# Performance work log

Measured on AMD Instinct MI355X. Metric: run time of the kernel, lower is better.

Reference implementation:

```python
import jax, jax.numpy as jnp
import numpy as np

B, N, D, DC, R = 32, 36, 2048, 4, 512  # batch, regions, feat dim, coord dim, fusion rank


def setup_inputs() -> dict:
    key = jax.random.key(0)
    ks = jax.random.split(key, 8)
    s = lambda fan_in: 1.0 / np.sqrt(fan_in)
    return {
        "mm": jax.random.normal(ks[0], (B, N, D), dtype=jnp.float32),
        "coords": jax.random.uniform(ks[1], (B, N, DC), dtype=jnp.float32),
        "U_feat": jax.random.normal(ks[2], (D, R), dtype=jnp.float32) * s(D),
        "V_feat": jax.random.normal(ks[3], (D, R), dtype=jnp.float32) * s(D),
        "P_feat": jax.random.normal(ks[4], (R, D), dtype=jnp.float32) * s(R),
        "U_coord": jax.random.normal(ks[5], (DC, R), dtype=jnp.float32) * s(DC),
        "V_coord": jax.random.normal(ks[6], (DC, R), dtype=jnp.float32) * s(DC),
        "P_coord": jax.random.normal(ks[7], (R, D), dtype=jnp.float32) * s(R),
    }


def reference(mm, coords, U_feat, V_feat, P_feat, U_coord, V_coord, P_coord):
    # Pairwise module: build all (i, j) region pairs, fuse, max-aggregate over j.
    # Original torch code detach_()'s the gathered pair tensors -> stop_gradient here.
    mm_sg = jax.lax.stop_gradient(mm)
    coords_sg = jax.lax.stop_gradient(coords)

    # Coord fusion (MLB-style low-rank multiplicative fusion)
    uc = jnp.einsum("bnc,cr->bnr", coords_sg, U_coord)   # [B,N,R]
    vc = jnp.einsum("bnc,cr->bnr", coords_sg, V_coord)   # [B,N,R]
    zc = jax.nn.relu(uc[:, :, None, :] * vc[:, None, :, :])  # [B,N,N,R]
    Rij = jnp.einsum("bijr,rd->bijd", zc, P_coord)       # [B,N,N,D]

    # Feature fusion
    uf = jnp.einsum("bnd,dr->bnr", mm_sg, U_feat)
    vf = jnp.einsum("bnd,dr->bnr", mm_sg, V_feat)
    zf = jax.nn.relu(uf[:, :, None, :] * vf[:, None, :, :])  # [B,N,N,R]
    Rij = Rij + jnp.einsum("bijr,rd->bijd", zf, P_feat)  # [B,N,N,D]

    # agg['type'] == 'max': reduce over the second region axis (j)
    mm_new = jnp.max(Rij, axis=2)                        # [B,N,D]

    # residual
    return mm_new + mm
```

## Files before the change

kernel.cpp:

```cpp
#include <hip/hip_runtime.h>

#define BI    1152
#define NREG  36
#define DD    2048
#define RR    512
#define KK    1024
#define ZROWS (BI*NREG)
#define MBLK  144
#define NBLK  256
#define ABUF  (MBLK*32)
#define BBUF  (NBLK*32)
#define BUFE  (ABUF+BBUF)

typedef __bf16 bf16;
typedef __bf16 bf16x8 __attribute__((ext_vector_type(8)));
typedef __bf16 bf16x4 __attribute__((ext_vector_type(4)));
typedef float  f32x4  __attribute__((ext_vector_type(4)));

__device__ __forceinline__ void gl_lds16(const void* g, void* l) {
  __builtin_amdgcn_global_load_lds(
      (const __attribute__((address_space(1))) unsigned int*)g,
      (__attribute__((address_space(3))) unsigned int*)l, 16, 0, 0);
}

__global__ void k_prep(const float* __restrict__ mm, const float* __restrict__ coords,
                       const float* __restrict__ U_feat, const float* __restrict__ V_feat,
                       const float* __restrict__ P_feat, const float* __restrict__ U_coord,
                       const float* __restrict__ V_coord, const float* __restrict__ P_coord,
                       bf16* __restrict__ mmb, bf16* __restrict__ UT, bf16* __restrict__ VT,
                       bf16* __restrict__ PTt, float* __restrict__ uc, float* __restrict__ vc) {
  __shared__ float tile[32][33];
  int bid = blockIdx.x, tid = threadIdx.x;
  if (bid < 2304) {
    int i = bid * 256 + tid;
    float4 v = ((const float4*)mm)[i];
    bf16x4 o = {(bf16)v.x, (bf16)v.y, (bf16)v.z, (bf16)v.w};
    ((bf16x4*)mmb)[i] = o;
  } else if (bid < 4352) {
    int rel = bid - 2304;
    int zz = rel >> 10, rr = rel & 1023;
    int c0 = (rr & 15) * 32, r0 = (rr >> 4) * 32;
    const float* in = zz ? V_feat : U_feat;
    bf16* outp = zz ? VT : UT;
    int tx = tid & 31, ty = tid >> 5;
#pragma unroll
    for (int k = 0; k < 4; k++)
      tile[ty + 8 * k][tx] = in[(long)(r0 + ty + 8 * k) * 512 + c0 + tx];
    __syncthreads();
#pragma unroll
    for (int k = 0; k < 4; k++)
      outp[(long)(c0 + ty + 8 * k) * 2048 + r0 + tx] = (bf16)tile[tx][ty + 8 * k];
  } else if (bid < 6400) {
    int rel = bid - 4352;
    int zz = rel >> 10, rr = rel & 1023;
    int c0 = (rr & 63) * 32, r0 = (rr >> 6) * 32;
    const float* in = zz ? P_feat : P_coord;
    int koff = zz * 512;
    int tx = tid & 31, ty = tid >> 5;
#pragma unroll
    for (int k = 0; k < 4; k++)
      tile[ty + 8 * k][tx] = in[(long)(r0 + ty + 8 * k) * 2048 + c0 + tx];
    __syncthreads();
    int kc = (koff + r0) >> 5;
#pragma unroll
    for (int k = 0; k < 4; k++) {
      int d = c0 + ty + 8 * k;
      PTt[((long)kc * 2048 + d) * 32 + tx] = (bf16)tile[tx][ty + 8 * k];
    }
  } else {
    int g = bid - 6400;
    float c0 = coords[g * 4 + 0], c1 = coords[g * 4 + 1];
    float c2 = coords[g * 4 + 2], c3 = coords[g * 4 + 3];
#pragma unroll
    for (int i = 0; i < 2; i++) {
      int r = tid + i * 256;
      uc[g * RR + r] = c0 * U_coord[r] + c1 * U_coord[RR + r] + c2 * U_coord[2 * RR + r] + c3 * U_coord[3 * RR + r];
      vc[g * RR + r] = c0 * V_coord[r] + c1 * V_coord[RR + r] + c2 * V_coord[2 * RR + r] + c3 * V_coord[3 * RR + r];
    }
  }
}

__launch_bounds__(256)
__global__ void k_gemm_uv(const bf16* __restrict__ mmb, const bf16* __restrict__ UT,
                          const bf16* __restrict__ VT, float* __restrict__ uf,
                          float* __restrict__ vf) {
  __shared__ bf16 lds2[2][6144];
  const bf16* Bmat = blockIdx.z ? VT : UT;
  float* outp = blockIdx.z ? vf : uf;
  int m0 = blockIdx.x * 64, n0 = blockIdx.y * 128;
  int tid = threadIdx.x, wave = tid >> 6, lane = tid & 63;
  int l15 = lane & 15, qv = lane >> 4;
  int qp_c = qv ^ ((l15 >> 1) & 3);
  int qs = (lane & 3) ^ ((lane >> 3) & 3);

  const bf16* gA = mmb + (long)(m0 + wave * 16 + (lane >> 2)) * 2048 + qs * 8;
  const bf16* gB = Bmat + (long)(n0 + wave * 32 + (lane >> 2)) * 2048 + qs * 8;
  int lA = wave * 512;
  int lB = 2048 + wave * 1024;

  auto stage = [&](int buf, int k0) {
    bf16* db = &lds2[buf][0];
    gl_lds16(gA + k0, db + lA);
    gl_lds16(gB + k0, db + lB);
    gl_lds16(gB + 16 * 2048 + k0, db + lB + 512);
  };

  f32x4 acc[4][2] = {};
  stage(0, 0);
  for (int k0 = 0; k0 < 2048; k0 += 32) {
    int cur = (k0 >> 5) & 1;
    __syncthreads();
    if (k0 + 32 < 2048) stage(cur ^ 1, k0 + 32);
    bf16x8 a[4], b[2];
#pragma unroll
    for (int mt = 0; mt < 4; mt++)
      a[mt] = *(const bf16x8*)(&lds2[cur][0] + (mt * 16 + l15) * 32 + qp_c * 8);
#pragma unroll
    for (int nt = 0; nt < 2; nt++)
      b[nt] = *(const bf16x8*)(&lds2[cur][2048] + (wave * 32 + nt * 16 + l15) * 32 + qp_c * 8);
#pragma unroll
    for (int mt = 0; mt < 4; mt++)
#pragma unroll
      for (int nt = 0; nt < 2; nt++)
        acc[mt][nt] = __builtin_amdgcn_mfma_f32_16x16x32_bf16(a[mt], b[nt], acc[mt][nt], 0, 0, 0);
  }
#pragma unroll
  for (int mt = 0; mt < 4; mt++)
#pragma unroll
    for (int nt = 0; nt < 2; nt++)
#pragma unroll
      for (int r = 0; r < 4; r++) {
        int row = m0 + mt * 16 + qv * 4 + r;
        int col = n0 + wave * 32 + nt * 16 + l15;
        outp[(long)row * RR + col] = acc[mt][nt][r];
      }
}

__global__ void k_build_z(const float* __restrict__ uc, const float* __restrict__ vc,
                          const float* __restrict__ uf, const float* __restrict__ vf,
                          bf16* __restrict__ z) {
  __shared__ float uL[36 * 128];
  __shared__ float vL[36 * 128];
  int kq = blockIdx.x, b = blockIdx.y, tid = threadIdx.x;
  const float* usrc = (kq < 4) ? uc : uf;
  const float* vsrc = (kq < 4) ? vc : vf;
  int kb = (kq & 3) * 128;
  for (int i = tid; i < 1152; i += 256) {
    int row = i >> 5, kk = (i & 31) * 4;
    long src = (long)(b * 36 + row) * RR + kb + kk;
    *(float4*)&uL[row * 128 + kk] = *(const float4*)(usrc + src);
    *(float4*)&vL[row * 128 + kk] = *(const float4*)(vsrc + src);
  }
  __syncthreads();
  for (int c = tid; c < 41472; c += 256) {
    int kcl = c / 10368;
    int rem = c - kcl * 10368;
    int row = rem >> 3;
    int x4 = rem & 7;
    int gl = row / 36;
    int j = row - gl * 36;
    int kl = kcl * 32 + x4 * 4;
    float4 u4 = *(const float4*)&uL[gl * 128 + kl];
    float4 v4 = *(const float4*)&vL[j * 128 + kl];
    float x0 = fmaxf(u4.x * v4.x, 0.f), x1 = fmaxf(u4.y * v4.y, 0.f);
    float x2 = fmaxf(u4.z * v4.z, 0.f), x3 = fmaxf(u4.w * v4.w, 0.f);
    bf16x4 o = {(bf16)x0, (bf16)x1, (bf16)x2, (bf16)x3};
    int bi = b * 36 + gl;
    long rowp = (long)(bi >> 2) * 144 + j * 4 + (bi & 3);
    *(bf16x4*)(z + ((long)(kq * 4 + kcl) * ZROWS + rowp) * 32 + x4 * 4) = o;
  }
}

__launch_bounds__(256, 2)
__global__ void k_main(const bf16* __restrict__ z, const bf16* __restrict__ PTt,
                       const float* __restrict__ mm, float* __restrict__ out) {
  __shared__ bf16 lds[2 * BUFE];
  int bid = blockIdx.x;
  int x = bid & 7, t = bid >> 3;
  int dt = t & 7, go = (t >> 3) * 8 + x;
  int d0 = dt * NBLK;
  int tid = threadIdx.x, wave = tid >> 6, lane = tid & 63;
  int l15 = lane & 15, qv = lane >> 4;
  int qp_c = qv ^ ((l15 >> 1) & 3);

  int qs = (lane & 3) ^ ((lane >> 3) & 3);
  int lroff = (lane >> 2) * 32 + qs * 8;

  const bf16* gA = z + (long)go * ABUF + wave * 1024 + lroff;
  const bf16* gB = PTt + (long)d0 * 32 + wave * 2048 + lroff;
  int lA = wave * 1024;
  int lB = ABUF + wave * 2048;

  int sbuf = 0;
  auto stage = [&]() {
    bf16* db = lds + sbuf * BUFE;
    gl_lds16(gA, db + lA);
    gl_lds16(gA + 512, db + lA + 512);
    if (wave == 0) gl_lds16(gA + 4096, db + 4096);
    gl_lds16(gB, db + lB);
    gl_lds16(gB + 512, db + lB + 512);
    gl_lds16(gB + 1024, db + lB + 1024);
    gl_lds16(gB + 1536, db + lB + 1536);
    gA += (long)ZROWS * 32;
    gB += 2048L * 32;
    sbuf ^= 1;
  };

  f32x4 acc[9][4] = {};
  stage();
  for (int kc = 0; kc < 32; kc++) {
    __syncthreads();
    if (kc < 31) stage();
    const bf16* cur = lds + (kc & 1) * BUFE;
    bf16x8 b[4];
#pragma unroll
    for (int nt = 0; nt < 4; nt++)
      b[nt] = *(const bf16x8*)(cur + ABUF + (wave * 64 + nt * 16 + l15) * 32 + qp_c * 8);
#pragma unroll
    for (int mt = 0; mt < 9; mt++) {
      bf16x8 av = *(const bf16x8*)(cur + (mt * 16 + l15) * 32 + qp_c * 8);
#pragma unroll
      for (int nt = 0; nt < 4; nt++)
        acc[mt][nt] = __builtin_amdgcn_mfma_f32_16x16x32_bf16(av, b[nt], acc[mt][nt], 0, 0, 0);
    }
  }

#pragma unroll
  for (int nt = 0; nt < 4; nt++) {
    float mx[4];
#pragma unroll
    for (int r = 0; r < 4; r++) {
      mx[r] = acc[0][nt][r];
#pragma unroll
      for (int mt = 1; mt < 9; mt++) mx[r] = fmaxf(mx[r], acc[mt][nt][r]);
      mx[r] = fmaxf(mx[r], __shfl_xor(mx[r], 16, 64));
      mx[r] = fmaxf(mx[r], __shfl_xor(mx[r], 32, 64));
    }
    if (lane < 16) {
      int col = d0 + wave * 64 + nt * 16 + lane;
#pragma unroll
      for (int r = 0; r < 4; r++) {
        long oa = (long)(go * 4 + r) * DD + col;
        out[oa] = mx[r] + mm[oa];
      }
    }
  }
}

extern "C" void kernel_launch(void* const* d_in, const int* in_sizes, int n_in,
                              void* d_out, int out_size, void* d_ws, size_t ws_size,
                              hipStream_t stream) {
  const float* mm     = (const float*)d_in[0];
  const float* coords = (const float*)d_in[1];
  const float* U_feat = (const float*)d_in[2];
  const float* V_feat = (const float*)d_in[3];
  const float* P_feat = (const float*)d_in[4];
  const float* U_coord= (const float*)d_in[5];
  const float* V_coord= (const float*)d_in[6];
  const float* P_coord= (const float*)d_in[7];
  float* out = (float*)d_out;

  char* ws = (char*)d_ws;
  bf16* z   = (bf16*)(ws + 0);
  bf16* PTt = (bf16*)(ws + 84934656);
  bf16* mmb = (bf16*)(ws + 89128960);
  bf16* UT  = (bf16*)(ws + 93847552);
  bf16* VT  = (bf16*)(ws + 95944704);
  float* uf = (float*)(ws + 98041856);
  float* vf = (float*)(ws + 100401152);
  float* uc = (float*)(ws + 102760448);
  float* vc = (float*)(ws + 105119744);

  k_prep<<<dim3(7552), dim3(256), 0, stream>>>(mm, coords, U_feat, V_feat, P_feat,
                                               U_coord, V_coord, P_coord,
                                               mmb, UT, VT, PTt, uc, vc);
  k_gemm_uv<<<dim3(18, 4, 2), dim3(256), 0, stream>>>(mmb, UT, VT, uf, vf);
  k_build_z<<<dim3(8, 32), dim3(256), 0, stream>>>(uc, vc, uf, vf, z);
  k_main<<<dim3(2304), dim3(256), 0, stream>>>(z, PTt, mm, out);
}
```

Baseline: 259.7 us.

## Split-K uv GEMM, split z-build grid, load P operand directly to registers

The uv projection GEMM is split along K into two halves, which doubles its block count, and the partial sums are added when k_build_z loads them. k_build_z also gets a third grid dimension so each block writes half the z tiles. In k_main the B (P) operand is now read straight from global memory into registers instead of being staged through LDS, which cuts LDS use and LDS traffic. The cost is extra workspace and global reads for the partial sums, and B loads that go uncoalesced through the cache instead of through LDS.

Result: no change. 255.9 us (-1.5%).

```diff
diff --git a/kernel.cpp b/kernel.cpp
--- a/kernel.cpp
+++ b/kernel.cpp
@@ -9,8 +9,6 @@
 #define MBLK  144
 #define NBLK  256
 #define ABUF  (MBLK*32)
-#define BBUF  (NBLK*32)
-#define BUFE  (ABUF+BBUF)
 
 typedef __bf16 bf16;
 typedef __bf16 bf16x8 __attribute__((ext_vector_type(8)));
@@ -83,18 +81,21 @@
 __launch_bounds__(256)
 __global__ void k_gemm_uv(const bf16* __restrict__ mmb, const bf16* __restrict__ UT,
                           const bf16* __restrict__ VT, float* __restrict__ uf,
-                          float* __restrict__ vf) {
+                          float* __restrict__ vf, float* __restrict__ uf2,
+                          float* __restrict__ vf2) {
   __shared__ bf16 lds2[2][6144];
-  const bf16* Bmat = blockIdx.z ? VT : UT;
-  float* outp = blockIdx.z ? vf : uf;
+  int uv = blockIdx.z >> 1, kh = blockIdx.z & 1;
+  const bf16* Bmat = uv ? VT : UT;
+  float* outp = uv ? (kh ? vf2 : vf) : (kh ? uf2 : uf);
   int m0 = blockIdx.x * 64, n0 = blockIdx.y * 128;
+  int kbase = kh * 1024;
   int tid = threadIdx.x, wave = tid >> 6, lane = tid & 63;
   int l15 = lane & 15, qv = lane >> 4;
   int qp_c = qv ^ ((l15 >> 1) & 3);
   int qs = (lane & 3) ^ ((lane >> 3) & 3);
 
-  const bf16* gA = mmb + (long)(m0 + wave * 16 + (lane >> 2)) * 2048 + qs * 8;
-  const bf16* gB = Bmat + (long)(n0 + wave * 32 + (lane >> 2)) * 2048 + qs * 8;
+  const bf16* gA = mmb + (long)(m0 + wave * 16 + (lane >> 2)) * 2048 + kbase + qs * 8;
+  const bf16* gB = Bmat + (long)(n0 + wave * 32 + (lane >> 2)) * 2048 + kbase + qs * 8;
   int lA = wave * 512;
   int lB = 2048 + wave * 1024;
 
@@ -107,10 +108,10 @@
 
   f32x4 acc[4][2] = {};
   stage(0, 0);
-  for (int k0 = 0; k0 < 2048; k0 += 32) {
+  for (int k0 = 0; k0 < 1024; k0 += 32) {
     int cur = (k0 >> 5) & 1;
     __syncthreads();
-    if (k0 + 32 < 2048) stage(cur ^ 1, k0 + 32);
+    if (k0 + 32 < 1024) stage(cur ^ 1, k0 + 32);
     bf16x8 a[4], b[2];
 #pragma unroll
     for (int mt = 0; mt < 4; mt++)
@@ -138,21 +139,31 @@
 
 __global__ void k_build_z(const float* __restrict__ uc, const float* __restrict__ vc,
                           const float* __restrict__ uf, const float* __restrict__ vf,
+                          const float* __restrict__ uf2, const float* __restrict__ vf2,
                           bf16* __restrict__ z) {
   __shared__ float uL[36 * 128];
   __shared__ float vL[36 * 128];
   int kq = blockIdx.x, b = blockIdx.y, tid = threadIdx.x;
-  const float* usrc = (kq < 4) ? uc : uf;
-  const float* vsrc = (kq < 4) ? vc : vf;
   int kb = (kq & 3) * 128;
   for (int i = tid; i < 1152; i += 256) {
     int row = i >> 5, kk = (i & 31) * 4;
     long src = (long)(b * 36 + row) * RR + kb + kk;
-    *(float4*)&uL[row * 128 + kk] = *(const float4*)(usrc + src);
-    *(float4*)&vL[row * 128 + kk] = *(const float4*)(vsrc + src);
+    float4 u4, v4;
+    if (kq < 4) {
+      u4 = *(const float4*)(uc + src);
+      v4 = *(const float4*)(vc + src);
+    } else {
+      float4 a1 = *(const float4*)(uf + src), a2 = *(const float4*)(uf2 + src);
+      float4 b1 = *(const float4*)(vf + src), b2 = *(const float4*)(vf2 + src);
+      u4.x = a1.x + a2.x; u4.y = a1.y + a2.y; u4.z = a1.z + a2.z; u4.w = a1.w + a2.w;
+      v4.x = b1.x + b2.x; v4.y = b1.y + b2.y; v4.z = b1.z + b2.z; v4.w = b1.w + b2.w;
+    }
+    *(float4*)&uL[row * 128 + kk] = u4;
+    *(float4*)&vL[row * 128 + kk] = v4;
   }
   __syncthreads();
-  for (int c = tid; c < 41472; c += 256) {
+  int cbase = blockIdx.z * 20736;
+  for (int c = cbase + tid; c < cbase + 20736; c += 256) {
     int kcl = c / 10368;
     int rem = c - kcl * 10368;
     int row = rem >> 3;
@@ -174,7 +185,7 @@
 __launch_bounds__(256, 2)
 __global__ void k_main(const bf16* __restrict__ z, const bf16* __restrict__ PTt,
                        const float* __restrict__ mm, float* __restrict__ out) {
-  __shared__ bf16 lds[2 * BUFE];
+  __shared__ bf16 lds[2 * ABUF];
   int bid = blockIdx.x;
   int x = bid & 7, t = bid >> 3;
   int dt = t & 7, go = (t >> 3) * 8 + x;
@@ -182,46 +193,55 @@
   int tid = threadIdx.x, wave = tid >> 6, lane = tid & 63;
   int l15 = lane & 15, qv = lane >> 4;
   int qp_c = qv ^ ((l15 >> 1) & 3);
-
   int qs = (lane & 3) ^ ((lane >> 3) & 3);
   int lroff = (lane >> 2) * 32 + qs * 8;
 
   const bf16* gA = z + (long)go * ABUF + wave * 1024 + lroff;
-  const bf16* gB = PTt + (long)d0 * 32 + wave * 2048 + lroff;
   int lA = wave * 1024;
-  int lB = ABUF + wave * 2048;
-
-  int sbuf = 0;
-  auto stage = [&]() {
-    bf16* db = lds + sbuf * BUFE;
+  const bf16* gB = PTt + (long)(d0 + wave * 64 + l15) * 32 + qv * 8;
+
+  auto stageA = [&](int buf) {
+    bf16* db = lds + buf * ABUF;
     gl_lds16(gA, db + lA);
     gl_lds16(gA + 512, db + lA + 512);
     if (wave == 0) gl_lds16(gA + 4096, db + 4096);
-    gl_lds16(gB, db + lB);
-    gl_lds16(gB + 512, db + lB + 512);
-    gl_lds16(gB + 1024, db + lB + 1024);
-    gl_lds16(gB + 1536, db + lB + 1536);
     gA += (long)ZROWS * 32;
-    gB += 2048L * 32;
-    sbuf ^= 1;
   };
+  auto loadB = [&](int kc, bf16x8* b) {
+    const bf16* p = gB + (long)kc * (2048 * 32);
+#pragma unroll
+    for (int nt = 0; nt < 4; nt++)
+      b[nt] = *(const bf16x8*)(p + nt * 512);
+  };
 
   f32x4 acc[9][4] = {};
-  stage();
-  for (int kc = 0; kc < 32; kc++) {
-    __syncthreads();
-    if (kc < 31) stage();
-    const bf16* cur = lds + (kc & 1) * BUFE;
-    bf16x8 b[4];
-#pragma unroll
-    for (int nt = 0; nt < 4; nt++)
-      b[nt] = *(const bf16x8*)(cur + ABUF + (wave * 64 + nt * 16 + l15) * 32 + qp_c * 8);
-#pragma unroll
-    for (int mt = 0; mt < 9; mt++) {
-      bf16x8 av = *(const bf16x8*)(cur + (mt * 16 + l15) * 32 + qp_c * 8);
-#pragma unroll
-      for (int nt = 0; nt < 4; nt++)
-        acc[mt][nt] = __builtin_amdgcn_mfma_f32_16x16x32_bf16(av, b[nt], acc[mt][nt], 0, 0, 0);
+  bf16x8 b0[4], b1[4];
+  stageA(0);
+  loadB(0, b0);
+  for (int kc = 0; kc < 32; kc += 2) {
+    __syncthreads();
+    if (kc + 1 < 32) { stageA(1); loadB(kc + 1, b1); }
+    {
+      const bf16* cur = lds;
+#pragma unroll
+      for (int mt = 0; mt < 9; mt++) {
+        bf16x8 av = *(const bf16x8*)(cur + (mt * 16 + l15) * 32 + qp_c * 8);
+#pragma unroll
+        for (int nt = 0; nt < 4; nt++)
+          acc[mt][nt] = __builtin_amdgcn_mfma_f32_16x16x32_bf16(av, b0[nt], acc[mt][nt], 0, 0, 0);
+      }
+    }
+    __syncthreads();
+    if (kc + 2 < 32) { stageA(0); loadB(kc + 2, b0); }
+    {
+      const bf16* cur = lds + ABUF;
+#pragma unroll
+      for (int mt = 0; mt < 9; mt++) {
+        bf16x8 av = *(const bf16x8*)(cur + (mt * 16 + l15) * 32 + qp_c * 8);
+#pragma unroll
+        for (int nt = 0; nt < 4; nt++)
+          acc[mt][nt] = __builtin_amdgcn_mfma_f32_16x16x32_bf16(av, b1[nt], acc[mt][nt], 0, 0, 0);
+      }
     }
   }
 
@@ -270,11 +290,13 @@
   float* vf = (float*)(ws + 100401152);
   float* uc = (float*)(ws + 102760448);
   float* vc = (float*)(ws + 105119744);
+  float* uf2= (float*)(ws + 107479040);
+  float* vf2= (float*)(ws + 109838336);
 
   k_prep<<<dim3(7552), dim3(256), 0, stream>>>(mm, coords, U_feat, V_feat, P_feat,
                                                U_coord, V_coord, P_coord,
                                                mmb, UT, VT, PTt, uc, vc);
-  k_gemm_uv<<<dim3(18, 4, 2), dim3(256), 0, stream>>>(mmb, UT, VT, uf, vf);
-  k_build_z<<<dim3(8, 32), dim3(256), 0, stream>>>(uc, vc, uf, vf, z);
+  k_gemm_uv<<<dim3(18, 4, 4), dim3(256), 0, stream>>>(mmb, UT, VT, uf, vf, uf2, vf2);
+  k_build_z<<<dim3(8, 32, 2), dim3(256), 0, stream>>>(uc, vc, uf, vf, uf2, vf2, z);
   k_main<<<dim3(2304), dim3(256), 0, stream>>>(z, PTt, mm, out);
 }
```
